# Performance work log

Measured on AMD Instinct MI355X. Metric: run time of the kernel, lower is better.

## Reference

```python
import jax, jax.numpy as jnp
import numpy as np

B, DIM, HEADS, HD, H, W = 1, 256, 8, 32, 64, 64
MLP = int(DIM * 4.0)
EPS = 1e-5


def _ln(x, g, b):
    # LayerNorm over channel dim of NCHW (torch applies it on NHWC last dim)
    mu = x.mean(axis=1, keepdims=True)
    var = ((x - mu) ** 2).mean(axis=1, keepdims=True)
    return (x - mu) / jnp.sqrt(var + EPS) * g[None, :, None, None] + b[None, :, None, None]


def _c1(x, w, b):
    # 1x1 conv: w is [out, in]
    return jnp.einsum('bchw,oc->bohw', x, w) + b[None, :, None, None]


def _c3(x, w, b):
    y = jax.lax.conv_general_dilated(x, w, (1, 1), ((1, 1), (1, 1)),
                                     dimension_numbers=('NCHW', 'OIHW', 'NCHW'))
    return y + b[None, :, None, None]


def setup_inputs() -> dict:
    key = jax.random.key(0)
    ks = jax.random.split(key, 16)
    init = lambda k, s: jax.random.normal(k, s, jnp.float32) * 0.02
    d = {}
    d['rgb_feat'] = jax.random.normal(ks[0], (B, DIM, H, W), jnp.float32)
    d['dpt_feat'] = jax.random.normal(ks[1], (B, DIM, H, W), jnp.float32)
    d['x_dpt'] = jax.random.normal(ks[2], (B, 1, 1024, 1024), jnp.float32)
    d['wq'] = init(ks[3], (DIM, DIM)); d['bq'] = jnp.zeros((DIM,), jnp.float32)
    d['wk'] = init(ks[4], (DIM, DIM)); d['bk'] = jnp.zeros((DIM,), jnp.float32)
    d['wv'] = init(ks[5], (DIM, DIM)); d['bv'] = jnp.zeros((DIM,), jnp.float32)
    d['wo'] = init(ks[6], (DIM, DIM)); d['bo'] = jnp.zeros((DIM,), jnp.float32)
    d['g_rgb'] = jnp.ones((DIM,), jnp.float32); d['b_rgb'] = jnp.zeros((DIM,), jnp.float32)
    d['g_dpt'] = jnp.ones((DIM,), jnp.float32); d['b_dpt'] = jnp.zeros((DIM,), jnp.float32)
    d['g1'] = jnp.ones((DIM,), jnp.float32); d['b1'] = jnp.zeros((DIM,), jnp.float32)
    d['g2'] = jnp.ones((DIM,), jnp.float32); d['b2'] = jnp.zeros((DIM,), jnp.float32)
    d['w_mlp1'] = init(ks[7], (MLP, DIM)); d['b_mlp1'] = jnp.zeros((MLP,), jnp.float32)
    d['w_mlp2'] = init(ks[8], (DIM, MLP)); d['b_mlp2'] = jnp.zeros((DIM,), jnp.float32)
    d['w_de1'] = init(ks[9], (DIM, 1, 3, 3)); d['b_de1'] = jnp.zeros((DIM,), jnp.float32)
    d['w_de2'] = init(ks[10], (DIM, DIM)); d['b_de2'] = jnp.zeros((DIM,), jnp.float32)
    d['pos_emb'] = init(ks[11], (1, DIM, 1, 1))
    d['scale'] = jnp.sqrt(jnp.float32(HD))
    return d


def reference(rgb_feat, dpt_feat, x_dpt, wq, bq, wk, bk, wv, bv, wo, bo,
              g_rgb, b_rgb, g_dpt, b_dpt, g1, b1, g2, b2,
              w_mlp1, b_mlp1, w_mlp2, b_mlp2, w_de1, b_de1, w_de2, b_de2,
              pos_emb, scale):
    Bn, C, Hh, Ww = rgb_feat.shape
    n = Hh * Ww
    rgb_ln = _ln(rgb_feat, g_rgb, b_rgb)
    dpt_ln = _ln(dpt_feat, g_dpt, b_dpt)
    # depth positional embedding: bilinear downsample (align_corners=False) + conv3x3 + relu + conv1x1
    xd = jax.image.resize(x_dpt, (Bn, 1, Hh, Ww), method='bilinear', antialias=False)
    pe = _c1(jax.nn.relu(_c3(xd, w_de1, b_de1)), w_de2, b_de2)
    rgb_ln = rgb_ln + pos_emb + pe
    dpt_ln = dpt_ln + pos_emb + pe
    # QKV as [B, heads, head_dim, N]
    q = _c1(rgb_ln, wq, bq).reshape(Bn, HEADS, HD, n)
    k = _c1(dpt_ln, wk, bk).reshape(Bn, HEADS, HD, n)
    v = _c1(dpt_ln, wv, bv).reshape(Bn, HEADS, HD, n)
    scores = jnp.einsum('bhdn,bhdm->bhnm', q, k) / scale
    attn = jax.nn.softmax(scores, axis=-1)  # dropout is identity in eval
    fused = jnp.einsum('bhnm,bhdm->bhdn', attn, v).reshape(Bn, C, Hh, Ww)
    out = _c1(fused, wo, bo) + rgb_feat
    out_ln = _ln(out, g1, b1)
    h = jax.nn.gelu(_c1(out_ln, w_mlp1, b_mlp1), approximate=False)
    mlp_out = _c1(h, w_mlp2, b_mlp2)
    out2 = mlp_out + out_ln
    return _ln(out2, g2, b2)
```

## Files before the change

### kernel.cpp

```cpp
#include <hip/hip_runtime.h>
#include <hip/hip_bf16.h>
#include <math.h>

constexpr int NTOK = 4096;
constexpr int CDIM = 256;
constexpr int MLPD = 1024;
constexpr float EPS_LN = 1e-5f;

typedef __attribute__((ext_vector_type(8))) short bf16x8;
typedef __attribute__((ext_vector_type(4))) float floatx4;
typedef unsigned short u16;
typedef unsigned int u32;

__device__ __forceinline__ u16 f2bf(float x) {
    union { float f; u32 u; } v; v.f = x;
    u32 r = v.u + 0x7fff + ((v.u >> 16) & 1);
    return (u16)(r >> 16);
}
__device__ __forceinline__ float bf2f(u16 u) {
    union { u32 i; float f; } v; v.i = ((u32)u) << 16; return v.f;
}
__device__ __forceinline__ u32 pkbf(float a, float b) {
    __hip_bfloat162 h = __float22bfloat162_rn(make_float2(a, b));
    union { __hip_bfloat162 h; u32 u; } v; v.h = h; return v.u;
}
__device__ __forceinline__ float gelu_exact(float x) {
    return 0.5f * x * (1.0f + erff(x * 0.70710678118654752f));
}

__global__ __launch_bounds__(256) void k_prep(const float* __restrict__ rgb,
                                              float* __restrict__ rgbT,
                                              const float* __restrict__ dpt,
                                              float* __restrict__ dptT,
                                              const float* __restrict__ xdpt,
                                              const float* __restrict__ w3,
                                              const float* __restrict__ b3,
                                              u16* __restrict__ y,
                                              const float* __restrict__ wq,
                                              const float* __restrict__ wk,
                                              const float* __restrict__ wv,
                                              const float* __restrict__ wo,
                                              const float* __restrict__ wde2,
                                              const float* __restrict__ wm1,
                                              const float* __restrict__ wm2,
                                              u16* __restrict__ arena) {
    int blk = blockIdx.x;
    int t = threadIdx.x;
    if (blk < 512) {
        const float* in = (blk < 256) ? rgb : dpt;
        float* out = (blk < 256) ? rgbT : dptT;
        int tb = blk & 255;
        int c0 = (tb & 63) * 64, r0 = (tb >> 6) * 64;
        __shared__ float T[64][65];
        int rr = t >> 4, cc = (t & 15) * 4;
#pragma unroll
        for (int i = 0; i < 4; ++i) {
            int row = i * 16 + rr;
            float4 v = *(const float4*)(in + (size_t)(r0 + row) * NTOK + c0 + cc);
            T[row][cc] = v.x; T[row][cc + 1] = v.y; T[row][cc + 2] = v.z; T[row][cc + 3] = v.w;
        }
        __syncthreads();
#pragma unroll
        for (int i = 0; i < 4; ++i) {
            int a = i * 16 + rr;
            float4 v;
            v.x = T[cc][a]; v.y = T[cc + 1][a]; v.z = T[cc + 2][a]; v.w = T[cc + 3][a];
            *(float4*)(out + (size_t)(c0 + a) * CDIM + r0 + cc) = v;
        }
    } else if (blk < 768) {
        __shared__ float nb[3][18];
        int n0 = (blk - 512) * 16;
        int yy = n0 >> 6, x0 = n0 & 63;
        if (t < 54) {
            int r = t / 18, cc = t % 18;
            int sy = yy - 1 + r, sx = x0 - 1 + cc;
            float v = 0.f;
            if (sy >= 0 && sy < 64 && sx >= 0 && sx < 64) {
                int r0 = 16 * sy + 7, c0 = 16 * sx + 7;
                v = 0.25f * (xdpt[r0 * 1024 + c0] + xdpt[r0 * 1024 + c0 + 1] +
                             xdpt[(r0 + 1) * 1024 + c0] + xdpt[(r0 + 1) * 1024 + c0 + 1]);
            }
            nb[r][cc] = v;
        }
        __syncthreads();
        float wv9[9];
#pragma unroll
        for (int i = 0; i < 9; ++i) wv9[i] = w3[t * 9 + i];
        float bb = b3[t];
#pragma unroll
        for (int k = 0; k < 16; ++k) {
            float acc = bb;
#pragma unroll
            for (int r = 0; r < 3; ++r)
#pragma unroll
                for (int kx = 0; kx < 3; ++kx) acc += wv9[r * 3 + kx] * nb[r][k + kx];
            y[(size_t)(n0 + k) * CDIM + t] = f2bf(fmaxf(acc, 0.f));
        }
    } else {
        int e0 = (blk - 768) * 1024 + t * 4;
        const float* src; int off;
        if (e0 < 65536)       { src = wq;   off = 0; }
        else if (e0 < 131072) { src = wk;   off = 65536; }
        else if (e0 < 196608) { src = wv;   off = 131072; }
        else if (e0 < 262144) { src = wo;   off = 196608; }
        else if (e0 < 327680) { src = wde2; off = 262144; }
        else if (e0 < 589824) { src = wm1;  off = 327680; }
        else                  { src = wm2;  off = 589824; }
        float4 v = *(const float4*)(src + (e0 - off));
        uint2 o; o.x = pkbf(v.x, v.y); o.y = pkbf(v.z, v.w);
        *(uint2*)(arena + e0) = o;
    }
}

__global__ __launch_bounds__(256) void k_lnT(const void* __restrict__ xA,
                                             const float* __restrict__ gA,
                                             const float* __restrict__ bA,
                                             void* __restrict__ yA,
                                             const void* __restrict__ xB,
                                             const float* __restrict__ gB,
                                             const float* __restrict__ bB,
                                             void* __restrict__ yB,
                                             const u16* __restrict__ pe,
                                             const float* __restrict__ pos,
                                             int xf32) {
    const void* x; const float* g; const float* bb; void* y;
    if (blockIdx.y == 0) { x = xA; g = gA; bb = bA; y = yA; }
    else                 { x = xB; g = gB; bb = bB; y = yB; }
    int n = blockIdx.x * 4 + (threadIdx.x >> 6);
    int lane = threadIdx.x & 63;
    int c = lane * 4;
    float4 xv;
    if (xf32) {
        xv = *((const float4*)x + (size_t)n * 64 + lane);
    } else {
        ushort4 u = *((const ushort4*)x + (size_t)n * 64 + lane);
        xv = make_float4(bf2f(u.x), bf2f(u.y), bf2f(u.z), bf2f(u.w));
    }
    float s = xv.x + xv.y + xv.z + xv.w;
    float s2 = xv.x * xv.x + xv.y * xv.y + xv.z * xv.z + xv.w * xv.w;
#pragma unroll
    for (int off = 1; off < 64; off <<= 1) {
        s += __shfl_xor(s, off, 64);
        s2 += __shfl_xor(s2, off, 64);
    }
    float mu = s * (1.0f / 256.0f);
    float var = s2 * (1.0f / 256.0f) - mu * mu;
    float rsd = rsqrtf(var + EPS_LN);
    float4 g4 = *(const float4*)(g + c);
    float4 b4 = *(const float4*)(bb + c);
    float4 o;
    o.x = (xv.x - mu) * rsd * g4.x + b4.x;
    o.y = (xv.y - mu) * rsd * g4.y + b4.y;
    o.z = (xv.z - mu) * rsd * g4.z + b4.z;
    o.w = (xv.w - mu) * rsd * g4.w + b4.w;
    if (pe) {
        float4 p4 = *(const float4*)(pos + c);
        ushort4 pu = *((const ushort4*)pe + (size_t)n * 64 + lane);
        o.x += p4.x + bf2f(pu.x);
        o.y += p4.y + bf2f(pu.y);
        o.z += p4.z + bf2f(pu.z);
        o.w += p4.w + bf2f(pu.w);
    }
    ushort4 ou;
    ou.x = f2bf(o.x); ou.y = f2bf(o.y); ou.z = f2bf(o.z); ou.w = f2bf(o.w);
    *((ushort4*)y + (size_t)n * 64 + lane) = ou;
}

#define LDB 72
__global__ __launch_bounds__(256) void k_bmm(const u16* __restrict__ X0, const void* __restrict__ W0,
                                             const float* __restrict__ B0, void* __restrict__ Y0, int f0,
                                             const u16* __restrict__ X1, const void* __restrict__ W1,
                                             const float* __restrict__ B1, void* __restrict__ Y1, int f1,
                                             const u16* __restrict__ X2, const void* __restrict__ W2,
                                             const float* __restrict__ B2, void* __restrict__ Y2, int f2,
                                             const void* __restrict__ res, const float* __restrict__ scl,
                                             int M, int K) {
    const u16* X; const void* Wp; const float* bias; void* Yp; int flags;
    if (blockIdx.z == 0)      { X = X0; Wp = W0; bias = B0; Yp = Y0; flags = f0; }
    else if (blockIdx.z == 1) { X = X1; Wp = W1; bias = B1; Yp = Y1; flags = f1; }
    else                      { X = X2; Wp = W2; bias = B2; Yp = Y2; flags = f2; }
    __shared__ u16 Xs[2][64 * LDB];
    __shared__ u16 Ws[2][64 * LDB];
    int tid = threadIdx.x;
    int wid = tid >> 6, lane = tid & 63;
    int lo16 = lane & 15, quad = lane >> 4;
    int wy = wid & 1, wx = wid >> 1;
    int n0 = blockIdx.x * 64, m0 = blockIdx.y * 64;
    int srow = tid >> 2, sseg = tid & 3;

    floatx4 acc[2][2];
#pragma unroll
    for (int i = 0; i < 2; ++i)
#pragma unroll
        for (int j = 0; j < 2; ++j) acc[i][j] = floatx4{0.f, 0.f, 0.f, 0.f};

    for (int k0 = 0; k0 < K; k0 += 128) {
        uint4 xr[2][2], wb[2][2];
#pragma unroll
        for (int hf = 0; hf < 2; ++hf) {
            const u16* xp = X + (size_t)(n0 + srow) * K + k0 + hf * 64 + sseg * 16;
            xr[hf][0] = *(const uint4*)xp;
            xr[hf][1] = *(const uint4*)(xp + 8);
            if (flags & 32) {
                const u16* wp = (const u16*)Wp + (size_t)(m0 + srow) * K + k0 + hf * 64 + sseg * 16;
                wb[hf][0] = *(const uint4*)wp;
                wb[hf][1] = *(const uint4*)(wp + 8);
            } else {
                const float* wp = (const float*)Wp + (size_t)(m0 + srow) * K + k0 + hf * 64 + sseg * 16;
                float4 w0 = *(const float4*)wp;
                float4 w1 = *(const float4*)(wp + 4);
                float4 w2 = *(const float4*)(wp + 8);
                float4 w3 = *(const float4*)(wp + 12);
                wb[hf][0].x = pkbf(w0.x, w0.y); wb[hf][0].y = pkbf(w0.z, w0.w);
                wb[hf][0].z = pkbf(w1.x, w1.y); wb[hf][0].w = pkbf(w1.z, w1.w);
                wb[hf][1].x = pkbf(w2.x, w2.y); wb[hf][1].y = pkbf(w2.z, w2.w);
                wb[hf][1].z = pkbf(w3.x, w3.y); wb[hf][1].w = pkbf(w3.z, w3.w);
            }
        }
        if (k0) __syncthreads();
#pragma unroll
        for (int hf = 0; hf < 2; ++hf) {
            *(uint4*)&Xs[hf][srow * LDB + sseg * 16] = xr[hf][0];
            *(uint4*)&Xs[hf][srow * LDB + sseg * 16 + 8] = xr[hf][1];
            *(uint4*)&Ws[hf][srow * LDB + sseg * 16] = wb[hf][0];
            *(uint4*)&Ws[hf][srow * LDB + sseg * 16 + 8] = wb[hf][1];
        }
        __syncthreads();
#pragma unroll
        for (int hf = 0; hf < 2; ++hf) {
            const u16* As = (flags & 2) ? &Ws[hf][0] : &Xs[hf][0];
            const u16* Bs = (flags & 2) ? &Xs[hf][0] : &Ws[hf][0];
#pragma unroll
            for (int h = 0; h < 2; ++h) {
                int ko = h * 32 + quad * 8;
                bf16x8 a0 = *(const bf16x8*)&As[(wy * 32 + lo16) * LDB + ko];
                bf16x8 a1 = *(const bf16x8*)&As[(wy * 32 + 16 + lo16) * LDB + ko];
                bf16x8 b0 = *(const bf16x8*)&Bs[(wx * 32 + lo16) * LDB + ko];
                bf16x8 b1 = *(const bf16x8*)&Bs[(wx * 32 + 16 + lo16) * LDB + ko];
                acc[0][0] = __builtin_amdgcn_mfma_f32_16x16x32_bf16(a0, b0, acc[0][0], 0, 0, 0);
                acc[0][1] = __builtin_amdgcn_mfma_f32_16x16x32_bf16(a0, b1, acc[0][1], 0, 0, 0);
                acc[1][0] = __builtin_amdgcn_mfma_f32_16x16x32_bf16(a1, b0, acc[1][0], 0, 0, 0);
                acc[1][1] = __builtin_amdgcn_mfma_f32_16x16x32_bf16(a1, b1, acc[1][1], 0, 0, 0);
            }
        }
    }

    u16* Y = (u16*)Yp;
    if (flags & 2) {
#pragma unroll
        for (int i = 0; i < 2; ++i)
#pragma unroll
            for (int r = 0; r < 4; ++r) {
                int ch = m0 + wy * 32 + i * 16 + quad * 4 + r;
                float bb = bias[ch];
#pragma unroll
                for (int j = 0; j < 2; ++j) {
                    int tok = n0 + wx * 32 + j * 16 + lo16;
                    Y[(size_t)ch * NTOK + tok] = f2bf(acc[i][j][r] + bb);
                }
            }
    } else {
        float smul = (flags & 16) ? 1.4426950408889634f / scl[0] : 1.0f;
        float bj0 = bias[m0 + wx * 32 + lo16];
        float bj1 = bias[m0 + wx * 32 + 16 + lo16];
        const float* rf = (const float*)res;
        const u16* rb = (const u16*)res;
#pragma unroll
        for (int i = 0; i < 2; ++i)
#pragma unroll
            for (int j = 0; j < 2; ++j) {
                int ch = m0 + wx * 32 + j * 16 + lo16;
                float bb = j ? bj1 : bj0;
#pragma unroll
                for (int r = 0; r < 4; ++r) {
                    int tok = n0 + wy * 32 + i * 16 + quad * 4 + r;
                    float v = (acc[i][j][r] + bb) * smul;
                    if (flags & 1) v = gelu_exact(v);
                    if (flags & 4) v += rf[(size_t)tok * M + ch];
                    if (flags & 8) v += bf2f(rb[(size_t)tok * M + ch]);
                    if (flags & 64)
                        Y[((size_t)(ch >> 5) * NTOK + tok) * 32 + (ch & 31)] = f2bf(v);
                    else
                        Y[(size_t)tok * M + ch] = f2bf(v);
                }
            }
    }
}

#define LDP 36
__global__ __launch_bounds__(256, 4) void k_fattn(const u16* __restrict__ Qh,
                                                  const u16* __restrict__ Kh,
                                                  const u16* __restrict__ Vc,
                                                  u16* __restrict__ fused) {
    int h = blockIdx.y;
    int q0 = blockIdx.x * 32;
    int tid = threadIdx.x;
    int wid = tid >> 6, lane = tid & 63;
    int lo16 = lane & 15, quad = lane >> 4;

    __shared__ u16 Pt[4][32 * LDP];
    __shared__ float Ored[4][32][33];
    __shared__ float Lred[4][32];

    const u16* qb = Qh + ((size_t)h * NTOK + q0) * 32;
    bf16x8 bq0 = *(const bf16x8*)(qb + (size_t)lo16 * 32 + quad * 8);
    bf16x8 bq1 = *(const bf16x8*)(qb + (size_t)(16 + lo16) * 32 + quad * 8);

    const u16* kp = Kh + ((size_t)h * NTOK + wid * 1024) * 32;
    const u16* vp0 = Vc + ((size_t)(h * 32 + lo16)) * NTOK + wid * 1024;
    const u16* vp1 = vp0 + (size_t)16 * NTOK;

    u16* P = &Pt[wid][0];
    int prow0 = lo16 * LDP;
    int prow1 = (16 + lo16) * LDP;

    floatx4 o00 = {0.f, 0.f, 0.f, 0.f}, o01 = o00, o10 = o00, o11 = o00;
    float l0 = 0.f, l1 = 0.f;

    bf16x8 ak0c = *(const bf16x8*)(kp + (size_t)lo16 * 32 + quad * 8);
    bf16x8 ak1c = *(const bf16x8*)(kp + (size_t)(16 + lo16) * 32 + quad * 8);
    bf16x8 av0c = *(const bf16x8*)(vp0 + quad * 8);
    bf16x8 av1c = *(const bf16x8*)(vp1 + quad * 8);

    for (int kt = 0; kt < 32; ++kt) {
        floatx4 z = {0.f, 0.f, 0.f, 0.f};
        floatx4 s00 = __builtin_amdgcn_mfma_f32_16x16x32_bf16(ak0c, bq0, z, 0, 0, 0);
        floatx4 s01 = __builtin_amdgcn_mfma_f32_16x16x32_bf16(ak0c, bq1, z, 0, 0, 0);
        floatx4 s10 = __builtin_amdgcn_mfma_f32_16x16x32_bf16(ak1c, bq0, z, 0, 0, 0);
        floatx4 s11 = __builtin_amdgcn_mfma_f32_16x16x32_bf16(ak1c, bq1, z, 0, 0, 0);

        int ktn = (kt + 1) & 31;
        const u16* kn = kp + (size_t)ktn * 32 * 32;
        bf16x8 ak0n = *(const bf16x8*)(kn + (size_t)lo16 * 32 + quad * 8);
        bf16x8 ak1n = *(const bf16x8*)(kn + (size_t)(16 + lo16) * 32 + quad * 8);
        bf16x8 av0n = *(const bf16x8*)(vp0 + ktn * 32 + quad * 8);
        bf16x8 av1n = *(const bf16x8*)(vp1 + ktn * 32 + quad * 8);

#pragma unroll
        for (int r = 0; r < 4; ++r) {
            s00[r] = __builtin_amdgcn_exp2f(s00[r]);
            s10[r] = __builtin_amdgcn_exp2f(s10[r]);
            s01[r] = __builtin_amdgcn_exp2f(s01[r]);
            s11[r] = __builtin_amdgcn_exp2f(s11[r]);
            l0 += s00[r] + s10[r];
            l1 += s01[r] + s11[r];
        }
        uint2 w;
        w.x = pkbf(s00[0], s00[1]); w.y = pkbf(s00[2], s00[3]);
        *(uint2*)&P[prow0 + quad * 4] = w;
        w.x = pkbf(s10[0], s10[1]); w.y = pkbf(s10[2], s10[3]);
        *(uint2*)&P[prow0 + 16 + quad * 4] = w;
        w.x = pkbf(s01[0], s01[1]); w.y = pkbf(s01[2], s01[3]);
        *(uint2*)&P[prow1 + quad * 4] = w;
        w.x = pkbf(s11[0], s11[1]); w.y = pkbf(s11[2], s11[3]);
        *(uint2*)&P[prow1 + 16 + quad * 4] = w;

        bf16x8 bp0 = *(const bf16x8*)&P[prow0 + quad * 8];
        bf16x8 bp1 = *(const bf16x8*)&P[prow1 + quad * 8];

        o00 = __builtin_amdgcn_mfma_f32_16x16x32_bf16(av0c, bp0, o00, 0, 0, 0);
        o10 = __builtin_amdgcn_mfma_f32_16x16x32_bf16(av1c, bp0, o10, 0, 0, 0);
        o01 = __builtin_amdgcn_mfma_f32_16x16x32_bf16(av0c, bp1, o01, 0, 0, 0);
        o11 = __builtin_amdgcn_mfma_f32_16x16x32_bf16(av1c, bp1, o11, 0, 0, 0);

        ak0c = ak0n; ak1c = ak1n; av0c = av0n; av1c = av1n;
    }

    l0 += __shfl_xor(l0, 16, 64); l0 += __shfl_xor(l0, 32, 64);
    l1 += __shfl_xor(l1, 16, 64); l1 += __shfl_xor(l1, 32, 64);
    if (quad == 0) {
        Lred[wid][lo16] = l0;
        Lred[wid][16 + lo16] = l1;
    }
#pragma unroll
    for (int r = 0; r < 4; ++r) {
        Ored[wid][quad * 4 + r][lo16] = o00[r];
        Ored[wid][quad * 4 + r][16 + lo16] = o01[r];
        Ored[wid][16 + quad * 4 + r][lo16] = o10[r];
        Ored[wid][16 + quad * 4 + r][16 + lo16] = o11[r];
    }
    __syncthreads();

    int q = tid >> 3, dc = (tid & 7) * 4;
    float lt = Lred[0][q] + Lred[1][q] + Lred[2][q] + Lred[3][q];
    float inv = 1.0f / lt;
    float v[4];
#pragma unroll
    for (int i = 0; i < 4; ++i) {
        int d = dc + i;
        v[i] = (Ored[0][d][q] + Ored[1][d][q] + Ored[2][d][q] + Ored[3][d][q]) * inv;
    }
    uint2 ow;
    ow.x = pkbf(v[0], v[1]);
    ow.y = pkbf(v[2], v[3]);
    *(uint2*)(fused + (size_t)(q0 + q) * CDIM + h * 32 + dc) = ow;
}

__global__ __launch_bounds__(256) void k_lntr(const u16* __restrict__ x,
                                              const float* __restrict__ g,
                                              const float* __restrict__ b,
                                              float* __restrict__ out) {
    __shared__ float T[16][260];
    int n0 = blockIdx.x * 16;
    int t = threadIdx.x;
    int tk = t >> 4, seg = t & 15;
    float v[16];
    {
        const u16* p = x + (size_t)(n0 + tk) * CDIM + seg * 16;
        uint4 a = *(const uint4*)p;
        uint4 bq = *(const uint4*)(p + 8);
        u32 uu[8] = {a.x, a.y, a.z, a.w, bq.x, bq.y, bq.z, bq.w};
#pragma unroll
        for (int i = 0; i < 8; ++i) {
            v[2 * i] = bf2f((u16)(uu[i] & 0xffff));
            v[2 * i + 1] = bf2f((u16)(uu[i] >> 16));
        }
    }
    float s = 0.f, s2 = 0.f;
#pragma unroll
    for (int i = 0; i < 16; ++i) { s += v[i]; s2 += v[i] * v[i]; }
#pragma unroll
    for (int off = 1; off < 16; off <<= 1) {
        s += __shfl_xor(s, off, 64);
        s2 += __shfl_xor(s2, off, 64);
    }
    float mu = s * (1.0f / 256.0f);
    float var = s2 * (1.0f / 256.0f) - mu * mu;
    float rsd = rsqrtf(var + EPS_LN);
#pragma unroll
    for (int i = 0; i < 16; ++i) {
        int c = seg * 16 + i;
        T[tk][c] = (v[i] - mu) * rsd * g[c] + b[c];
    }
    __syncthreads();
    int c = t;
    float o[16];
#pragma unroll
    for (int j = 0; j < 16; ++j) o[j] = T[j][c];
    float* dst = out + (size_t)c * NTOK + n0;
#pragma unroll
    for (int j = 0; j < 4; ++j) {
        float4 w = {o[4 * j], o[4 * j + 1], o[4 * j + 2], o[4 * j + 3]};
        *(float4*)(dst + 4 * j) = w;
    }
}

extern "C" void kernel_launch(void* const* d_in, const int* in_sizes, int n_in,
                              void* d_out, int out_size, void* d_ws, size_t ws_size,
                              hipStream_t stream) {
    const float* rgb    = (const float*)d_in[0];
    const float* dpt    = (const float*)d_in[1];
    const float* x_dpt  = (const float*)d_in[2];
    const float* wq     = (const float*)d_in[3];
    const float* bq     = (const float*)d_in[4];
    const float* wk     = (const float*)d_in[5];
    const float* bk     = (const float*)d_in[6];
    const float* wv     = (const float*)d_in[7];
    const float* bv     = (const float*)d_in[8];
    const float* wo     = (const float*)d_in[9];
    const float* bo     = (const float*)d_in[10];
    const float* g_rgb  = (const float*)d_in[11];
    const float* b_rgb  = (const float*)d_in[12];
    const float* g_dpt  = (const float*)d_in[13];
    const float* b_dpt  = (const float*)d_in[14];
    const float* g1     = (const float*)d_in[15];
    const float* b1     = (const float*)d_in[16];
    const float* g2     = (const float*)d_in[17];
    const float* b2     = (const float*)d_in[18];
    const float* w_mlp1 = (const float*)d_in[19];
    const float* b_mlp1 = (const float*)d_in[20];
    const float* w_mlp2 = (const float*)d_in[21];
    const float* b_mlp2 = (const float*)d_in[22];
    const float* w_de1  = (const float*)d_in[23];
    const float* b_de1  = (const float*)d_in[24];
    const float* w_de2  = (const float*)d_in[25];
    const float* b_de2  = (const float*)d_in[26];
    const float* pos    = (const float*)d_in[27];
    const float* scale  = (const float*)d_in[28];
    float* out = (float*)d_out;

    char* base = (char*)d_ws;
    const size_t MB = 1u << 20;
    float* rgbT    = (float*)(base + 0 * MB);
    float* dptT    = (float*)(base + 4 * MB);
    u16*   outT    = (u16*)(base + 4 * MB);
    u16*   out_lnT = (u16*)(base + 6 * MB);
    u16*   relu3T  = (u16*)(base + 8 * MB);
    u16*   hT      = (u16*)(base + 8 * MB);
    u16*   peT     = (u16*)(base + 10 * MB);
    u16*   aqT     = (u16*)(base + 12 * MB);
    u16*   akvT    = (u16*)(base + 14 * MB);
    u16*   Qhm     = (u16*)(base + 16 * MB);
    u16*   out2T   = (u16*)(base + 16 * MB);
    u16*   Khm     = (u16*)(base + 18 * MB);
    u16*   Vcm     = (u16*)(base + 20 * MB);
    u16*   fusedT  = (u16*)(base + 22 * MB);
    u16*   arena   = (u16*)(base + 24 * MB);

    bool aw = ws_size >= 26 * MB;
    int wf = aw ? 32 : 0;
    const void* Wq  = aw ? (const void*)(arena + 0)      : (const void*)wq;
    const void* Wk  = aw ? (const void*)(arena + 65536)  : (const void*)wk;
    const void* Wv  = aw ? (const void*)(arena + 131072) : (const void*)wv;
    const void* Wo  = aw ? (const void*)(arena + 196608) : (const void*)wo;
    const void* Wd2 = aw ? (const void*)(arena + 262144) : (const void*)w_de2;
    const void* Wm1 = aw ? (const void*)(arena + 327680) : (const void*)w_mlp1;
    const void* Wm2 = aw ? (const void*)(arena + 589824) : (const void*)w_mlp2;

    k_prep<<<aw ? 512 + 256 + 832 : 512 + 256, 256, 0, stream>>>(
        rgb, rgbT, dpt, dptT, x_dpt, w_de1, b_de1, relu3T,
        wq, wk, wv, wo, w_de2, w_mlp1, w_mlp2, arena);
    k_bmm<<<dim3(64, 4, 1), 256, 0, stream>>>(relu3T, Wd2, b_de2, peT, wf,
                                              nullptr, nullptr, nullptr, nullptr, 0,
                                              nullptr, nullptr, nullptr, nullptr, 0,
                                              nullptr, nullptr, CDIM, CDIM);
    k_lnT<<<dim3(1024, 2), 256, 0, stream>>>(rgbT, g_rgb, b_rgb, aqT,
                                             dptT, g_dpt, b_dpt, akvT,
                                             peT, pos, 1);
    k_bmm<<<dim3(64, 4, 3), 256, 0, stream>>>(aqT, Wq, bq, Qhm, wf | 16 | 64,
                                              akvT, Wk, bk, Khm, wf | 64,
                                              akvT, Wv, bv, Vcm, wf | 2,
                                              nullptr, scale, CDIM, CDIM);
    k_fattn<<<dim3(128, 8), 256, 0, stream>>>(Qhm, Khm, Vcm, fusedT);
    k_bmm<<<dim3(64, 4, 1), 256, 0, stream>>>(fusedT, Wo, bo, outT, wf | 4,
                                              nullptr, nullptr, nullptr, nullptr, 0,
                                              nullptr, nullptr, nullptr, nullptr, 0,
                                              rgbT, nullptr, CDIM, CDIM);
    k_lnT<<<dim3(1024, 1), 256, 0, stream>>>(outT, g1, b1, out_lnT,
                                             nullptr, nullptr, nullptr, nullptr,
                                             nullptr, nullptr, 0);
    k_bmm<<<dim3(64, 16, 1), 256, 0, stream>>>(out_lnT, Wm1, b_mlp1, hT, wf | 1,
                                               nullptr, nullptr, nullptr, nullptr, 0,
                                               nullptr, nullptr, nullptr, nullptr, 0,
                                               nullptr, nullptr, MLPD, CDIM);
    k_bmm<<<dim3(64, 4, 1), 256, 0, stream>>>(hT, Wm2, b_mlp2, out2T, wf | 8,
                                              nullptr, nullptr, nullptr, nullptr, 0,
                                              nullptr, nullptr, nullptr, nullptr, 0,
                                              out_lnT, nullptr, CDIM, MLPD);
    k_lntr<<<256, 256, 0, stream>>>(out2T, g2, b2, out);
}
```

Baseline: 249.6 us.

## Split K across two thread groups in GEMM and widen attention to 8 waves

The GEMM kernel now runs 512 threads, with two 256-thread groups each covering half of K in 64-wide steps. The partial accumulators are combined through shared memory before the epilogue, which roughly doubles the waves in flight for these small GEMMs. The flash-attention kernel moves from 4 to 8 waves per block, each wave handling 512 keys instead of 1024, and the cross-wave reduction grows to 8 partials. The trade-offs are single-buffered LDS staging with two barriers per step, a larger shared-memory footprint in attention (the Ored array doubles), and lost occupancy hints from the launch bounds.

```diff
diff --git a/kernel.cpp b/kernel.cpp
--- a/kernel.cpp
+++ b/kernel.cpp
@@ -167,7 +167,7 @@
 }
 
 #define LDB 72
-__global__ __launch_bounds__(256) void k_bmm(const u16* __restrict__ X0, const void* __restrict__ W0,
+__global__ __launch_bounds__(512) void k_bmm(const u16* __restrict__ X0, const void* __restrict__ W0,
                                              const float* __restrict__ B0, void* __restrict__ Y0, int f0,
                                              const u16* __restrict__ X1, const void* __restrict__ W1,
                                              const float* __restrict__ B1, void* __restrict__ Y1, int f1,
@@ -181,12 +181,18 @@
     else                      { X = X2; Wp = W2; bias = B2; Yp = Y2; flags = f2; }
     __shared__ u16 Xs[2][64 * LDB];
     __shared__ u16 Ws[2][64 * LDB];
+    float* Cred = (float*)&Xs[0][0];
+
     int tid = threadIdx.x;
-    int wid = tid >> 6, lane = tid & 63;
+    int kg = tid >> 8;
+    int t = tid & 255;
+    int wid = t >> 6, lane = t & 63;
     int lo16 = lane & 15, quad = lane >> 4;
     int wy = wid & 1, wx = wid >> 1;
     int n0 = blockIdx.x * 64, m0 = blockIdx.y * 64;
-    int srow = tid >> 2, sseg = tid & 3;
+    int srow = t >> 2, sseg = t & 3;
+    int Khalf = K >> 1;
+    int kbase = kg * Khalf;
 
     floatx4 acc[2][2];
 #pragma unroll
@@ -194,55 +200,70 @@
 #pragma unroll
         for (int j = 0; j < 2; ++j) acc[i][j] = floatx4{0.f, 0.f, 0.f, 0.f};
 
-    for (int k0 = 0; k0 < K; k0 += 128) {
-        uint4 xr[2][2], wb[2][2];
-#pragma unroll
-        for (int hf = 0; hf < 2; ++hf) {
-            const u16* xp = X + (size_t)(n0 + srow) * K + k0 + hf * 64 + sseg * 16;
-            xr[hf][0] = *(const uint4*)xp;
-            xr[hf][1] = *(const uint4*)(xp + 8);
-            if (flags & 32) {
-                const u16* wp = (const u16*)Wp + (size_t)(m0 + srow) * K + k0 + hf * 64 + sseg * 16;
-                wb[hf][0] = *(const uint4*)wp;
-                wb[hf][1] = *(const uint4*)(wp + 8);
-            } else {
-                const float* wp = (const float*)Wp + (size_t)(m0 + srow) * K + k0 + hf * 64 + sseg * 16;
-                float4 w0 = *(const float4*)wp;
-                float4 w1 = *(const float4*)(wp + 4);
-                float4 w2 = *(const float4*)(wp + 8);
-                float4 w3 = *(const float4*)(wp + 12);
-                wb[hf][0].x = pkbf(w0.x, w0.y); wb[hf][0].y = pkbf(w0.z, w0.w);
-                wb[hf][0].z = pkbf(w1.x, w1.y); wb[hf][0].w = pkbf(w1.z, w1.w);
-                wb[hf][1].x = pkbf(w2.x, w2.y); wb[hf][1].y = pkbf(w2.z, w2.w);
-                wb[hf][1].z = pkbf(w3.x, w3.y); wb[hf][1].w = pkbf(w3.z, w3.w);
-            }
-        }
-        if (k0) __syncthreads();
-#pragma unroll
-        for (int hf = 0; hf < 2; ++hf) {
-            *(uint4*)&Xs[hf][srow * LDB + sseg * 16] = xr[hf][0];
-            *(uint4*)&Xs[hf][srow * LDB + sseg * 16 + 8] = xr[hf][1];
-            *(uint4*)&Ws[hf][srow * LDB + sseg * 16] = wb[hf][0];
-            *(uint4*)&Ws[hf][srow * LDB + sseg * 16 + 8] = wb[hf][1];
+    for (int k0 = 0; k0 < Khalf; k0 += 64) {
+        int kk = kbase + k0;
+        const u16* xp = X + (size_t)(n0 + srow) * K + kk + sseg * 16;
+        uint4 xr0 = *(const uint4*)xp;
+        uint4 xr1 = *(const uint4*)(xp + 8);
+        uint4 wb0, wb1;
+        if (flags & 32) {
+            const u16* wp = (const u16*)Wp + (size_t)(m0 + srow) * K + kk + sseg * 16;
+            wb0 = *(const uint4*)wp;
+            wb1 = *(const uint4*)(wp + 8);
+        } else {
+            const float* wp = (const float*)Wp + (size_t)(m0 + srow) * K + kk + sseg * 16;
+            float4 w0 = *(const float4*)wp;
+            float4 w1 = *(const float4*)(wp + 4);
+            float4 w2 = *(const float4*)(wp + 8);
+            float4 w3 = *(const float4*)(wp + 12);
+            wb0.x = pkbf(w0.x, w0.y); wb0.y = pkbf(w0.z, w0.w);
+            wb0.z = pkbf(w1.x, w1.y); wb0.w = pkbf(w1.z, w1.w);
+            wb1.x = pkbf(w2.x, w2.y); wb1.y = pkbf(w2.z, w2.w);
+            wb1.z = pkbf(w3.x, w3.y); wb1.w = pkbf(w3.z, w3.w);
         }
         __syncthreads();
-#pragma unroll
-        for (int hf = 0; hf < 2; ++hf) {
-            const u16* As = (flags & 2) ? &Ws[hf][0] : &Xs[hf][0];
-            const u16* Bs = (flags & 2) ? &Xs[hf][0] : &Ws[hf][0];
-#pragma unroll
-            for (int h = 0; h < 2; ++h) {
-                int ko = h * 32 + quad * 8;
-                bf16x8 a0 = *(const bf16x8*)&As[(wy * 32 + lo16) * LDB + ko];
-                bf16x8 a1 = *(const bf16x8*)&As[(wy * 32 + 16 + lo16) * LDB + ko];
-                bf16x8 b0 = *(const bf16x8*)&Bs[(wx * 32 + lo16) * LDB + ko];
-                bf16x8 b1 = *(const bf16x8*)&Bs[(wx * 32 + 16 + lo16) * LDB + ko];
-                acc[0][0] = __builtin_amdgcn_mfma_f32_16x16x32_bf16(a0, b0, acc[0][0], 0, 0, 0);
-                acc[0][1] = __builtin_amdgcn_mfma_f32_16x16x32_bf16(a0, b1, acc[0][1], 0, 0, 0);
-                acc[1][0] = __builtin_amdgcn_mfma_f32_16x16x32_bf16(a1, b0, acc[1][0], 0, 0, 0);
-                acc[1][1] = __builtin_amdgcn_mfma_f32_16x16x32_bf16(a1, b1, acc[1][1], 0, 0, 0);
-            }
-        }
+        *(uint4*)&Xs[kg][srow * LDB + sseg * 16] = xr0;
+        *(uint4*)&Xs[kg][srow * LDB + sseg * 16 + 8] = xr1;
+        *(uint4*)&Ws[kg][srow * LDB + sseg * 16] = wb0;
+        *(uint4*)&Ws[kg][srow * LDB + sseg * 16 + 8] = wb1;
+        __syncthreads();
+
+        const u16* As = (flags & 2) ? &Ws[kg][0] : &Xs[kg][0];
+        const u16* Bs = (flags & 2) ? &Xs[kg][0] : &Ws[kg][0];
+#pragma unroll
+        for (int h = 0; h < 2; ++h) {
+            int ko = h * 32 + quad * 8;
+            bf16x8 a0 = *(const bf16x8*)&As[(wy * 32 + lo16) * LDB + ko];
+            bf16x8 a1 = *(const bf16x8*)&As[(wy * 32 + 16 + lo16) * LDB + ko];
+            bf16x8 b0 = *(const bf16x8*)&Bs[(wx * 32 + lo16) * LDB + ko];
+            bf16x8 b1 = *(const bf16x8*)&Bs[(wx * 32 + 16 + lo16) * LDB + ko];
+            acc[0][0] = __builtin_amdgcn_mfma_f32_16x16x32_bf16(a0, b0, acc[0][0], 0, 0, 0);
+            acc[0][1] = __builtin_amdgcn_mfma_f32_16x16x32_bf16(a0, b1, acc[0][1], 0, 0, 0);
+            acc[1][0] = __builtin_amdgcn_mfma_f32_16x16x32_bf16(a1, b0, acc[1][0], 0, 0, 0);
+            acc[1][1] = __builtin_amdgcn_mfma_f32_16x16x32_bf16(a1, b1, acc[1][1], 0, 0, 0);
+        }
+    }
+
+    __syncthreads();
+    if (kg == 1) {
+        float* c = &Cred[t * 17];
+#pragma unroll
+        for (int i = 0; i < 2; ++i)
+#pragma unroll
+            for (int j = 0; j < 2; ++j)
+#pragma unroll
+                for (int r = 0; r < 4; ++r) c[(i * 2 + j) * 4 + r] = acc[i][j][r];
+    }
+    __syncthreads();
+    if (kg == 1) return;
+    {
+        const float* c = &Cred[t * 17];
+#pragma unroll
+        for (int i = 0; i < 2; ++i)
+#pragma unroll
+            for (int j = 0; j < 2; ++j)
+#pragma unroll
+                for (int r = 0; r < 4; ++r) acc[i][j][r] += c[(i * 2 + j) * 4 + r];
     }
 
     u16* Y = (u16*)Yp;
@@ -288,31 +309,30 @@
 }
 
 #define LDP 36
-__global__ __launch_bounds__(256, 4) void k_fattn(const u16* __restrict__ Qh,
-                                                  const u16* __restrict__ Kh,
-                                                  const u16* __restrict__ Vc,
-                                                  u16* __restrict__ fused) {
+__global__ __launch_bounds__(512) void k_fattn(const u16* __restrict__ Qh,
+                                               const u16* __restrict__ Kh,
+                                               const u16* __restrict__ Vc,
+                                               u16* __restrict__ fused) {
     int h = blockIdx.y;
     int q0 = blockIdx.x * 32;
     int tid = threadIdx.x;
     int wid = tid >> 6, lane = tid & 63;
     int lo16 = lane & 15, quad = lane >> 4;
 
-    __shared__ u16 Pt[4][32 * LDP];
-    __shared__ float Ored[4][32][33];
-    __shared__ float Lred[4][32];
+    __shared__ u16 Pt[8][32 * LDP];
+    __shared__ float Ored[8][32][33];
+    __shared__ float Lred[8][32];
 
     const u16* qb = Qh + ((size_t)h * NTOK + q0) * 32;
     bf16x8 bq0 = *(const bf16x8*)(qb + (size_t)lo16 * 32 + quad * 8);
     bf16x8 bq1 = *(const bf16x8*)(qb + (size_t)(16 + lo16) * 32 + quad * 8);
 
-    const u16* kp = Kh + ((size_t)h * NTOK + wid * 1024) * 32;
-    const u16* vp0 = Vc + ((size_t)(h * 32 + lo16)) * NTOK + wid * 1024;
+    const u16* kp = Kh + ((size_t)h * NTOK + wid * 512) * 32;
+    const u16* vp0 = Vc + ((size_t)(h * 32 + lo16)) * NTOK + wid * 512;
     const u16* vp1 = vp0 + (size_t)16 * NTOK;
 
     u16* P = &Pt[wid][0];
-    int prow0 = lo16 * LDP;
-    int prow1 = (16 + lo16) * LDP;
+    int prow0 = lo16 * LDP, prow1 = (16 + lo16) * LDP;
 
     floatx4 o00 = {0.f, 0.f, 0.f, 0.f}, o01 = o00, o10 = o00, o11 = o00;
     float l0 = 0.f, l1 = 0.f;
@@ -322,14 +342,14 @@
     bf16x8 av0c = *(const bf16x8*)(vp0 + quad * 8);
     bf16x8 av1c = *(const bf16x8*)(vp1 + quad * 8);
 
-    for (int kt = 0; kt < 32; ++kt) {
+    for (int kt = 0; kt < 16; ++kt) {
         floatx4 z = {0.f, 0.f, 0.f, 0.f};
         floatx4 s00 = __builtin_amdgcn_mfma_f32_16x16x32_bf16(ak0c, bq0, z, 0, 0, 0);
         floatx4 s01 = __builtin_amdgcn_mfma_f32_16x16x32_bf16(ak0c, bq1, z, 0, 0, 0);
         floatx4 s10 = __builtin_amdgcn_mfma_f32_16x16x32_bf16(ak1c, bq0, z, 0, 0, 0);
         floatx4 s11 = __builtin_amdgcn_mfma_f32_16x16x32_bf16(ak1c, bq1, z, 0, 0, 0);
 
-        int ktn = (kt + 1) & 31;
+        int ktn = (kt + 1) & 15;
         const u16* kn = kp + (size_t)ktn * 32 * 32;
         bf16x8 ak0n = *(const bf16x8*)(kn + (size_t)lo16 * 32 + quad * 8);
         bf16x8 ak1n = *(const bf16x8*)(kn + (size_t)(16 + lo16) * 32 + quad * 8);
@@ -381,19 +401,18 @@
     }
     __syncthreads();
 
-    int q = tid >> 3, dc = (tid & 7) * 4;
-    float lt = Lred[0][q] + Lred[1][q] + Lred[2][q] + Lred[3][q];
+    int q = tid >> 4, d0 = (tid & 15) * 2;
+    float lt = 0.f;
+#pragma unroll
+    for (int wv = 0; wv < 8; ++wv) lt += Lred[wv][q];
     float inv = 1.0f / lt;
-    float v[4];
-#pragma unroll
-    for (int i = 0; i < 4; ++i) {
-        int d = dc + i;
-        v[i] = (Ored[0][d][q] + Ored[1][d][q] + Ored[2][d][q] + Ored[3][d][q]) * inv;
-    }
-    uint2 ow;
-    ow.x = pkbf(v[0], v[1]);
-    ow.y = pkbf(v[2], v[3]);
-    *(uint2*)(fused + (size_t)(q0 + q) * CDIM + h * 32 + dc) = ow;
+    float v0 = 0.f, v1 = 0.f;
+#pragma unroll
+    for (int wv = 0; wv < 8; ++wv) {
+        v0 += Ored[wv][d0][q];
+        v1 += Ored[wv][d0 + 1][q];
+    }
+    *(u32*)(fused + (size_t)(q0 + q) * CDIM + h * 32 + d0) = pkbf(v0 * inv, v1 * inv);
 }
 
 __global__ __launch_bounds__(256) void k_lntr(const u16* __restrict__ x,
@@ -510,30 +529,30 @@
     k_prep<<<aw ? 512 + 256 + 832 : 512 + 256, 256, 0, stream>>>(
         rgb, rgbT, dpt, dptT, x_dpt, w_de1, b_de1, relu3T,
         wq, wk, wv, wo, w_de2, w_mlp1, w_mlp2, arena);
-    k_bmm<<<dim3(64, 4, 1), 256, 0, stream>>>(relu3T, Wd2, b_de2, peT, wf,
+    k_bmm<<<dim3(64, 4, 1), 512, 0, stream>>>(relu3T, Wd2, b_de2, peT, wf,
                                               nullptr, nullptr, nullptr, nullptr, 0,
                                               nullptr, nullptr, nullptr, nullptr, 0,
                                               nullptr, nullptr, CDIM, CDIM);
     k_lnT<<<dim3(1024, 2), 256, 0, stream>>>(rgbT, g_rgb, b_rgb, aqT,
                                              dptT, g_dpt, b_dpt, akvT,
                                              peT, pos, 1);
-    k_bmm<<<dim3(64, 4, 3), 256, 0, stream>>>(aqT, Wq, bq, Qhm, wf | 16 | 64,
+    k_bmm<<<dim3(64, 4, 3), 512, 0, stream>>>(aqT, Wq, bq, Qhm, wf | 16 | 64,
                                               akvT, Wk, bk, Khm, wf | 64,
                                               akvT, Wv, bv, Vcm, wf | 2,
                                               nullptr, scale, CDIM, CDIM);
-    k_fattn<<<dim3(128, 8), 256, 0, stream>>>(Qhm, Khm, Vcm, fusedT);
-    k_bmm<<<dim3(64, 4, 1), 256, 0, stream>>>(fusedT, Wo, bo, outT, wf | 4,
+    k_fattn<<<dim3(128, 8), 512, 0, stream>>>(Qhm, Khm, Vcm, fusedT);
+    k_bmm<<<dim3(64, 4, 1), 512, 0, stream>>>(fusedT, Wo, bo, outT, wf | 4,
                                               nullptr, nullptr, nullptr, nullptr, 0,
                                               nullptr, nullptr, nullptr, nullptr, 0,
                                               rgbT, nullptr, CDIM, CDIM);
     k_lnT<<<dim3(1024, 1), 256, 0, stream>>>(outT, g1, b1, out_lnT,
                                              nullptr, nullptr, nullptr, nullptr,
                                              nullptr, nullptr, 0);
-    k_bmm<<<dim3(64, 16, 1), 256, 0, stream>>>(out_lnT, Wm1, b_mlp1, hT, wf | 1,
+    k_bmm<<<dim3(64, 16, 1), 512, 0, stream>>>(out_lnT, Wm1, b_mlp1, hT, wf | 1,
                                                nullptr, nullptr, nullptr, nullptr, 0,
                                                nullptr, nullptr, nullptr, nullptr, 0,
                                                nullptr, nullptr, MLPD, CDIM);
-    k_bmm<<<dim3(64, 4, 1), 256, 0, stream>>>(hT, Wm2, b_mlp2, out2T, wf | 8,
+    k_bmm<<<dim3(64, 4, 1), 512, 0, stream>>>(hT, Wm2, b_mlp2, out2T, wf | 8,
                                               nullptr, nullptr, nullptr, nullptr, 0,
                                               nullptr, nullptr, nullptr, nullptr, 0,
                                               out_lnT, nullptr, CDIM, MLPD);
```

Result: faster. 224.9 us (-9.9%).
